# Kernel optimization log

Measured on AMD Instinct MI355X. Metric: run time of the kernel, lower is better.

Reference implementation:

```python
import jax, jax.numpy as jnp
import numpy as np

N = 100000      # nodes per graph-batch
E = 1600000     # edges per graph-batch (avg degree 16)
G = 64          # graphs per batch (segments for mean pool)
DIN = 128
DH = 128


def setup_inputs() -> dict:
    key = jax.random.key(0)
    ks = jax.random.split(key, 14)
    x0 = jax.random.normal(ks[0], (N, DIN), jnp.float32)
    x1 = jax.random.normal(ks[1], (N, DIN), jnp.float32)
    edge_index0 = jax.random.randint(ks[2], (2, E), 0, N)
    edge_index1 = jax.random.randint(ks[3], (2, E), 0, N)
    batch0 = jnp.sort(jax.random.randint(ks[4], (N,), 0, G))
    batch1 = jnp.sort(jax.random.randint(ks[5], (N,), 0, G))
    s = 0.05
    W1 = jax.random.normal(ks[6], (DIN, DH), jnp.float32) * s
    b1 = jnp.zeros((DH,), jnp.float32)
    W2 = jax.random.normal(ks[7], (DH, DH), jnp.float32) * s
    b2 = jnp.zeros((DH,), jnp.float32)
    Wc1 = jax.random.normal(ks[8], (2 * DH, DH), jnp.float32) * s
    bc1 = jnp.zeros((DH,), jnp.float32)
    Wc2 = jax.random.normal(ks[9], (DH, 1), jnp.float32) * s
    bc2 = jnp.zeros((1,), jnp.float32)
    return dict(x0=x0, x1=x1, edge_index0=edge_index0, edge_index1=edge_index1,
                batch0=batch0, batch1=batch1,
                W1=W1, b1=b1, W2=W2, b2=b2, Wc1=Wc1, bc1=bc1, Wc2=Wc2, bc2=bc2)


def gcn_conv(x, edge_index, W, b):
    # PyG GCNConv: add self-loops, symmetric norm D^-1/2 (A+I) D^-1/2, then XW + b
    n = x.shape[0]
    sl = jnp.arange(n)
    src = jnp.concatenate([edge_index[0], sl])
    dst = jnp.concatenate([edge_index[1], sl])
    ones = jnp.ones(src.shape[0], x.dtype)
    deg = jax.ops.segment_sum(ones, dst, num_segments=n)
    dinv = jnp.where(deg > 0, jax.lax.rsqrt(deg), 0.0)
    norm = dinv[src] * dinv[dst]               # [E+N]
    h = x @ W                                   # [N, DH]
    msg = h[src] * norm[:, None]                # gather + scale
    return jax.ops.segment_sum(msg, dst, num_segments=n) + b


def graph_embedding(x, edge_index, batch, W1, b1, W2, b2):
    f = gcn_conv(x, edge_index, W1, b1)
    # dropout is identity in eval mode
    f = gcn_conv(f, edge_index, W2, b2)
    s = jax.ops.segment_sum(f, batch, num_segments=G)
    cnt = jax.ops.segment_sum(jnp.ones((f.shape[0],), f.dtype), batch, num_segments=G)
    return s / jnp.maximum(cnt, 1.0)[:, None]   # global_mean_pool -> [G, DH]


def reference(x0, x1, edge_index0, edge_index1, batch0, batch1,
              W1, b1, W2, b2, Wc1, bc1, Wc2, bc2):
    f0 = graph_embedding(x0, edge_index0, batch0, W1, b1, W2, b2)
    f1 = graph_embedding(x1, edge_index1, batch1, W1, b1, W2, b2)
    c = jnp.concatenate([f0, f1], axis=1)       # [G, 2*DH]
    h = jax.nn.sigmoid(c @ Wc1 + bc1)
    prob = jax.nn.sigmoid(h @ Wc2 + bc2)
    return prob[:, 0]                           # squeeze(-1) -> [G]
```

## Files before the change

### kernel.cpp

```cpp
#include <hip/hip_runtime.h>
#include <hip/hip_bf16.h>

#define NN 100000
#define NE 1600000
#define NG 64
#define DHID 128
#define PB 32
#define NBUCK 196
#define CAPE 10240
#define CHUNK 8192

#if __has_builtin(__builtin_amdgcn_cvt_pk_f32_fp8) && __has_builtin(__builtin_amdgcn_cvt_pk_fp8_f32)
#define FP8_HW 1
#endif

typedef float f32x2 __attribute__((ext_vector_type(2)));
typedef float f32x4 __attribute__((ext_vector_type(4)));
typedef short bf16x8 __attribute__((ext_vector_type(8)));

__device__ __forceinline__ float fp8_dec_sw(unsigned b) {
    unsigned u = ((b & 0x80u) << 24) | ((b & 0x7fu) << 20);
    return __uint_as_float(u) * 0x1p+120f;
}
__device__ __forceinline__ unsigned fp8_enc_sw(float f) {
    unsigned s = (__float_as_uint(f) >> 24) & 0x80u;
    float af = fabsf(f);
    if (!(af > 0x1p-10f)) return s;
    if (af > 448.f) af = 448.f;
    int e; float m = frexpf(af, &e);
    int ee = e + 6;
    unsigned bits;
    if (ee <= 0) {
        int k = (int)rintf(af * 512.0f);
        if (k > 7) k = 7;
        bits = (unsigned)k;
    } else {
        int mm = (int)rintf(m * 16.0f);
        if (mm == 16) { mm = 8; ee += 1; }
        if (ee > 15) { ee = 15; mm = 14; }
        bits = ((unsigned)ee << 3) | (unsigned)(mm - 8);
    }
    return s | bits;
}

__device__ __forceinline__ unsigned short fp8_pack2(float a, float b) {
#ifdef FP8_HW
    return (unsigned short)__builtin_amdgcn_cvt_pk_fp8_f32(a, b, 0, false);
#else
    return (unsigned short)(fp8_enc_sw(a) | (fp8_enc_sw(b) << 8));
#endif
}

__device__ __forceinline__ void fp8_acc4(unsigned u, float& a0, float& a1, float& a2, float& a3) {
#ifdef FP8_HW
    f32x2 lo = __builtin_amdgcn_cvt_pk_f32_fp8((int)u, false);
    f32x2 hi = __builtin_amdgcn_cvt_pk_f32_fp8((int)u, true);
    a0 += lo[0]; a1 += lo[1]; a2 += hi[0]; a3 += hi[1];
#else
    a0 += fp8_dec_sw(u & 0xffu);
    a1 += fp8_dec_sw((u >> 8) & 0xffu);
    a2 += fp8_dec_sw((u >> 16) & 0xffu);
    a3 += fp8_dec_sw(u >> 24);
#endif
}

__device__ __forceinline__ unsigned short f2bf(float f) {
    unsigned u = __float_as_uint(f);
    return (unsigned short)((u + 0x7FFFu + ((u >> 16) & 1u)) >> 16);
}


__global__ void initcur_kernel(int* __restrict__ cursor) {
    int i = blockIdx.x * 256 + threadIdx.x;
    if (i < 2 * NBUCK) cursor[i] = i * CAPE;
}

__global__ __launch_bounds__(256) void bin_kernel(const int* __restrict__ ei0, const int* __restrict__ ei1,
                                                  int* __restrict__ cursor,
                                                  unsigned int* __restrict__ binned, int E, int nch) {
    __shared__ int hist[256], scn[256], lofs[256], lcur[256], basex[256];
    __shared__ unsigned int stage[CHUNK];
    __shared__ unsigned char stageB[CHUNK];
    int g = blockIdx.x / nch;
    int ch = blockIdx.x - g * nch;
    const int* ei = g ? ei1 : ei0;
    int* cur = cursor + g * NBUCK;
    int t = threadIdx.x;
    int c0 = ch * CHUNK;
    int cend = min(c0 + CHUNK, E);
    hist[t] = 0;
    __syncthreads();
    for (int e = c0 + t; e < cend; e += 256)
        atomicAdd(&hist[((unsigned)ei[E + e]) >> 9], 1);
    __syncthreads();
    scn[t] = hist[t];
    __syncthreads();
    for (int off = 1; off < 256; off <<= 1) {
        int v = (t >= off) ? scn[t - off] : 0;
        __syncthreads();
        scn[t] += v;
        __syncthreads();
    }
    int excl = scn[t] - hist[t];
    lofs[t] = excl;
    lcur[t] = excl;
    if (hist[t] > 0) basex[t] = atomicAdd(&cur[t], hist[t]);
    __syncthreads();
    for (int e = c0 + t; e < cend; e += 256) {
        int dst = ei[E + e], src = ei[e];
        int b = ((unsigned)dst) >> 9;
        int r = atomicAdd(&lcur[b], 1);
        stage[r]  = (((unsigned)(dst & 511)) << 17) | (unsigned)src;
        stageB[r] = (unsigned char)b;
    }
    __syncthreads();
    int cnt = cend - c0;
    for (int i = t; i < cnt; i += 256) {
        int b = stageB[i];
        binned[basex[b] + (i - lofs[b])] = stage[i];
    }
}

__global__ __launch_bounds__(256) void fine_kernel(int* __restrict__ cursor,
                                                   unsigned int* __restrict__ binned,
                                                   float* __restrict__ dinv, int2* __restrict__ rng) {
    __shared__ unsigned int stage[CAPE];
    __shared__ int hist[512], ofs[512], lcur[512];
    __shared__ int pscan[256];
    int bb = blockIdx.x;
    int g = bb / NBUCK, bl = bb - g * NBUCK;
    int t = threadIdx.x;
    int gbase = bb * CAPE;
    int cnt = min(cursor[bb] - gbase, CAPE);
    for (int i = t; i < cnt; i += 256) stage[i] = binned[gbase + i];
    hist[t] = 0; hist[t + 256] = 0;
    __syncthreads();
    for (int i = t; i < cnt; i += 256) atomicAdd(&hist[stage[i] >> 17], 1);
    __syncthreads();
    int a0 = hist[2 * t], a1 = hist[2 * t + 1];
    pscan[t] = a0 + a1;
    __syncthreads();
    for (int off = 1; off < 256; off <<= 1) {
        int v = (t >= off) ? pscan[t - off] : 0;
        __syncthreads();
        pscan[t] += v;
        __syncthreads();
    }
    int pex = pscan[t] - (a0 + a1);
    ofs[2 * t] = pex;       ofs[2 * t + 1] = pex + a0;
    lcur[2 * t] = pex;      lcur[2 * t + 1] = pex + a0;
    __syncthreads();
#pragma unroll
    for (int q = 0; q < 2; ++q) {
        int l = t + 256 * q;
        int node = bl * 512 + l;
        if (node < NN) {
            int dg = hist[l];
            dinv[(size_t)g * NN + node] = rsqrtf((float)(dg + 1));
            rng[(size_t)g * NN + node] = make_int2(gbase + ofs[l], gbase + ofs[l] + dg);
        }
    }
    for (int i = t; i < cnt; i += 256) {
        unsigned int p = stage[i];
        int l = p >> 17;
        int r = atomicAdd(&lcur[l], 1);
        binned[gbase + r] = p & 0x1FFFFu;
    }
    if (t == 0) cursor[bb] = gbase;
}


__global__ void bounds_kernel(const int* __restrict__ b0, const int* __restrict__ b1,
                              int* __restrict__ bounds, int n) {
    int t = threadIdx.x;
    int gb = t >> 6, j = t & 63;
    const int* b = gb ? b1 : b0;
    int lo = 0, hi = n;
    while (lo < hi) { int mid = (lo + hi) >> 1; if (b[mid] < j) lo = mid + 1; else hi = mid; }
    bounds[gb * 65 + j] = lo;
    if (j == 0) bounds[gb * 65 + 64] = n;
}


__global__ __launch_bounds__(256) void wpack_kernel(const float* __restrict__ W1, const float* __restrict__ W2,
                                                    unsigned short* __restrict__ Wp1, unsigned short* __restrict__ Wp2) {
    int o = blockIdx.x * 256 + threadIdx.x;
    const float* W = (o < 16384) ? W1 : W2;
    unsigned short* Wp = (o < 16384) ? Wp1 : Wp2;
    int oo = o & 16383;
    int j = oo & 7, l = (oo >> 3) & 63, tile = oo >> 9;
    int kt = tile >> 3, ct = tile & 7;
    int k = kt * 32 + ((l >> 4) << 3) + j;
    int c = ct * 16 + (l & 15);
    Wp[oo] = f2bf(W[k * 128 + c]);
}


template<bool BF16IN>
__global__ __launch_bounds__(256) void gemm_mfma(const void* __restrict__ Avoid,
                                                 const unsigned short* __restrict__ Wp,
                                                 const float* __restrict__ dinv,
                                                 unsigned int* __restrict__ Hs8dw, int n) {
    int wave = threadIdx.x >> 6, lane = threadIdx.x & 63;
    int row_base = blockIdx.x * 64 + wave * 16;
    int r = lane & 15, kg = lane >> 4;
    int rowc = min(row_base + r, n - 1);

    bf16x8 af[4];
    if (BF16IN) {
        const uint4* A = (const uint4*)Avoid;
#pragma unroll
        for (int kt = 0; kt < 4; ++kt) {
            uint4 p = A[(size_t)rowc * 16 + kt * 4 + kg];
            af[kt] = *(bf16x8*)&p;
        }
    } else {
        const float4* A = (const float4*)Avoid;
#pragma unroll
        for (int kt = 0; kt < 4; ++kt) {
            float4 p0 = A[(size_t)rowc * 32 + kt * 8 + kg * 2];
            float4 p1 = A[(size_t)rowc * 32 + kt * 8 + kg * 2 + 1];
            bf16x8 a;
            a[0] = (short)f2bf(p0.x); a[1] = (short)f2bf(p0.y);
            a[2] = (short)f2bf(p0.z); a[3] = (short)f2bf(p0.w);
            a[4] = (short)f2bf(p1.x); a[5] = (short)f2bf(p1.y);
            a[6] = (short)f2bf(p1.z); a[7] = (short)f2bf(p1.w);
            af[kt] = a;
        }
    }

    f32x4 acc[8] = {};
    const bf16x8* Wf = (const bf16x8*)Wp;
#pragma unroll
    for (int kt = 0; kt < 4; ++kt) {
#pragma unroll
        for (int ct = 0; ct < 8; ++ct) {
            bf16x8 bf = Wf[(kt * 8 + ct) * 64 + lane];
            acc[ct] = __builtin_amdgcn_mfma_f32_16x16x32_bf16(af[kt], bf, acc[ct], 0, 0, 0);
        }
    }

    float dvr[4]; bool rok[4]; int erow[4];
#pragma unroll
    for (int reg = 0; reg < 4; ++reg) {
        erow[reg] = row_base + ((lane >> 4) << 2) + reg;
        rok[reg] = erow[reg] < n;
        dvr[reg] = dinv[min(erow[reg], n - 1)];
    }
#pragma unroll
    for (int ct = 0; ct < 8; ++ct) {
#pragma unroll
        for (int reg = 0; reg < 4; ++reg) {
            float v = acc[ct][reg] * dvr[reg];
            float v1 = __shfl_xor(v, 1);
            unsigned us = fp8_pack2(v, v1);
            unsigned u2 = (unsigned)__shfl_xor((int)us, 2);
            if ((lane & 3) == 0 && rok[reg]) {
                unsigned dword = (us & 0xffffu) | (u2 << 16);
                Hs8dw[(size_t)erow[reg] * 32 + ct * 4 + ((lane & 15) >> 2)] = dword;
            }
        }
    }
}


__global__ __launch_bounds__(256) void conv_gather(const unsigned int* __restrict__ Hs8,
                                                   const int2* __restrict__ rng,
                                                   const int* __restrict__ csr, const float* __restrict__ dinv,
                                                   const float* __restrict__ bias, uint2* __restrict__ out16, int n) {
    int wave = blockIdx.x * 4 + (threadIdx.x >> 6);
    int lane = threadIdx.x & 63;
    if (wave >= n) return;
    int d = wave;
    int half = lane >> 5;
    int h = lane & 31;
    int2 se = rng[d];
    int k0 = se.x, k1 = se.y;
    float a0 = 0.f, a1 = 0.f, a2 = 0.f, a3 = 0.f;
    int k = k0 + half;
    for (; k + 14 < k1; k += 16) {
        int s0 = csr[k],      s1 = csr[k + 2],  s2 = csr[k + 4],  s3 = csr[k + 6];
        int s4 = csr[k + 8],  s5 = csr[k + 10], s6 = csr[k + 12], s7 = csr[k + 14];
        unsigned u0 = Hs8[(size_t)s0 * 32 + h];
        unsigned u1 = Hs8[(size_t)s1 * 32 + h];
        unsigned u2 = Hs8[(size_t)s2 * 32 + h];
        unsigned u3 = Hs8[(size_t)s3 * 32 + h];
        unsigned u4 = Hs8[(size_t)s4 * 32 + h];
        unsigned u5 = Hs8[(size_t)s5 * 32 + h];
        unsigned u6 = Hs8[(size_t)s6 * 32 + h];
        unsigned u7 = Hs8[(size_t)s7 * 32 + h];
        fp8_acc4(u0, a0, a1, a2, a3);
        fp8_acc4(u1, a0, a1, a2, a3);
        fp8_acc4(u2, a0, a1, a2, a3);
        fp8_acc4(u3, a0, a1, a2, a3);
        fp8_acc4(u4, a0, a1, a2, a3);
        fp8_acc4(u5, a0, a1, a2, a3);
        fp8_acc4(u6, a0, a1, a2, a3);
        fp8_acc4(u7, a0, a1, a2, a3);
    }
    for (; k + 6 < k1; k += 8) {
        int s0 = csr[k], s1 = csr[k + 2], s2 = csr[k + 4], s3 = csr[k + 6];
        unsigned u0 = Hs8[(size_t)s0 * 32 + h];
        unsigned u1 = Hs8[(size_t)s1 * 32 + h];
        unsigned u2 = Hs8[(size_t)s2 * 32 + h];
        unsigned u3 = Hs8[(size_t)s3 * 32 + h];
        fp8_acc4(u0, a0, a1, a2, a3);
        fp8_acc4(u1, a0, a1, a2, a3);
        fp8_acc4(u2, a0, a1, a2, a3);
        fp8_acc4(u3, a0, a1, a2, a3);
    }
    for (; k < k1; k += 2) {
        unsigned u = Hs8[(size_t)csr[k] * 32 + h];
        fp8_acc4(u, a0, a1, a2, a3);
    }
    if (half == 0) {
        unsigned ud = Hs8[(size_t)d * 32 + h];
        fp8_acc4(ud, a0, a1, a2, a3);
    }
    a0 += __shfl_xor(a0, 32);
    a1 += __shfl_xor(a1, 32);
    a2 += __shfl_xor(a2, 32);
    a3 += __shfl_xor(a3, 32);
    if (half == 0) {
        float dv = dinv[d];
        float4 b = ((const float4*)bias)[h];
        unsigned short w0 = f2bf(fmaf(a0, dv, b.x));
        unsigned short w1 = f2bf(fmaf(a1, dv, b.y));
        unsigned short w2 = f2bf(fmaf(a2, dv, b.z));
        unsigned short w3 = f2bf(fmaf(a3, dv, b.w));
        uint2 o;
        o.x = (unsigned)w0 | ((unsigned)w1 << 16);
        o.y = (unsigned)w2 | ((unsigned)w3 << 16);
        out16[(size_t)d * 32 + h] = o;
    }
}


__global__ __launch_bounds__(256) void pool_part(const unsigned int* __restrict__ F16,
                                                 const int* __restrict__ bounds,
                                                 float* __restrict__ partial) {
    __shared__ float sh[512];
    int g   = blockIdx.x / PB;
    int sub = blockIdx.x % PB;
    int s = bounds[g], e = bounds[g + 1];
    int len = e - s;
    int chunk = (len + PB - 1) / PB;
    int is = s + sub * chunk;
    int ie = min(is + chunk, e);
    int cp = threadIdx.x & 63;
    int quarter = threadIdx.x >> 6;
    float acc0 = 0.f, acc1 = 0.f;
    for (int i = is + quarter; i < ie; i += 4) {
        unsigned u = F16[(size_t)i * 64 + cp];
        acc0 += __uint_as_float(u << 16);
        acc1 += __uint_as_float(u & 0xffff0000u);
    }
    sh[threadIdx.x] = acc0;
    sh[threadIdx.x + 256] = acc1;
    __syncthreads();
    if (threadIdx.x < 64) {
        float m0 = sh[cp] + sh[64 + cp] + sh[128 + cp] + sh[192 + cp];
        float m1 = sh[256 + cp] + sh[320 + cp] + sh[384 + cp] + sh[448 + cp];
        partial[((size_t)g * PB + sub) * 128 + 2 * cp]     = m0;
        partial[((size_t)g * PB + sub) * 128 + 2 * cp + 1] = m1;
    }
}


__global__ __launch_bounds__(128) void pool_finish(const float* __restrict__ partial, const int* __restrict__ bounds,
                                                   float* __restrict__ pool) {
    int gg = blockIdx.x;
    int gb = gg >> 6, g = gg & 63;
    int col = threadIdx.x;
    const float* p = partial + ((size_t)gb * NG + g) * PB * 128;
    float acc = 0.f;
#pragma unroll
    for (int sub = 0; sub < PB; ++sub) acc += p[sub * 128 + col];
    int len = bounds[gb * 65 + g + 1] - bounds[gb * 65 + g];
    pool[(size_t)gg * 128 + col] = acc / fmaxf((float)len, 1.0f);
}


__global__ __launch_bounds__(128) void classifier_kernel(const float* __restrict__ pool,
                                                         const float* __restrict__ Wc1, const float* __restrict__ bc1,
                                                         const float* __restrict__ Wc2, const float* __restrict__ bc2,
                                                         float* __restrict__ out) {
    __shared__ float sh[128];
    int g = blockIdx.x;
    int j = threadIdx.x;
    float acc = bc1[j];
    const float* p0 = pool + (size_t)g * 128;
    const float* p1 = pool + (size_t)(NG + g) * 128;
    for (int k = 0; k < 128; ++k) acc = fmaf(p0[k], Wc1[k * 128 + j], acc);
    for (int k = 0; k < 128; ++k) acc = fmaf(p1[k], Wc1[(128 + k) * 128 + j], acc);
    float h = 1.0f / (1.0f + expf(-acc));
    sh[j] = h * Wc2[j];
    __syncthreads();
    for (int off = 64; off > 0; off >>= 1) {
        if (j < off) sh[j] += sh[j + off];
        __syncthreads();
    }
    if (j == 0) out[g] = 1.0f / (1.0f + expf(-(sh[0] + bc2[0])));
}


extern "C" void kernel_launch(void* const* d_in, const int* in_sizes, int n_in,
                              void* d_out, int out_size, void* d_ws, size_t ws_size,
                              hipStream_t stream) {
    const float* x[2]     = {(const float*)d_in[0], (const float*)d_in[1]};
    const int*   ei[2]    = {(const int*)d_in[2], (const int*)d_in[3]};
    const int*   batch[2] = {(const int*)d_in[4], (const int*)d_in[5]};
    const float* W1  = (const float*)d_in[6];
    const float* b1  = (const float*)d_in[7];
    const float* W2  = (const float*)d_in[8];
    const float* b2  = (const float*)d_in[9];
    const float* Wc1 = (const float*)d_in[10];
    const float* bc1 = (const float*)d_in[11];
    const float* Wc2 = (const float*)d_in[12];
    const float* bc2 = (const float*)d_in[13];
    float* out = (float*)d_out;

    char* w = (char*)d_ws;
    unsigned short*  buf16  = (unsigned short*)w;  w += (size_t)NN * DHID * 2;
    unsigned short*  hs     = (unsigned short*)w;  w += (size_t)NN * DHID;
    unsigned int*    binned = (unsigned int*)w;    w += (size_t)2 * NBUCK * CAPE * 4;
    int2*            rng    = (int2*)w;            w += (size_t)2 * NN * 8;
    float*           dinv   = (float*)w;           w += (size_t)2 * NN * 4;
    unsigned short*  wp1    = (unsigned short*)w;  w += (size_t)128 * 128 * 2;
    unsigned short*  wp2    = (unsigned short*)w;  w += (size_t)128 * 128 * 2;
    int*             cursor = (int*)w;             w += (size_t)2 * NBUCK * 4 + 16;
    int*             bounds = (int*)w;             w += 2 * 65 * 4 + 8;
    float*           partial= (float*)w;           w += (size_t)2 * NG * PB * DHID * 4;
    float*           pool   = (float*)w;           w += (size_t)2 * NG * DHID * 4;

    if ((size_t)(w - (char*)d_ws) > ws_size) return;

    const int nch = (NE + CHUNK - 1) / CHUNK;

    bounds_kernel<<<1, 128, 0, stream>>>(batch[0], batch[1], bounds, NN);
    wpack_kernel<<<128, 256, 0, stream>>>(W1, W2, wp1, wp2);
    initcur_kernel<<<2, 256, 0, stream>>>(cursor);

    bin_kernel<<<2 * nch, 256, 0, stream>>>(ei[0], ei[1], cursor, binned, NE, nch);
    fine_kernel<<<2 * NBUCK, 256, 0, stream>>>(cursor, binned, dinv, rng);

    const int gemm_grid = (NN + 63) / 64;

    for (int g = 0; g < 2; ++g) {
        const float* dv = dinv + (size_t)g * NN;
        const int2*  rg = rng + (size_t)g * NN;

        gemm_mfma<false><<<gemm_grid, 256, 0, stream>>>(x[g], wp1, dv, (unsigned int*)hs, NN);
        conv_gather<<<(NN + 3) / 4, 256, 0, stream>>>((const unsigned int*)hs, rg, (const int*)binned, dv, b1, (uint2*)buf16, NN);
        gemm_mfma<true><<<gemm_grid, 256, 0, stream>>>(buf16, wp2, dv, (unsigned int*)hs, NN);
        conv_gather<<<(NN + 3) / 4, 256, 0, stream>>>((const unsigned int*)hs, rg, (const int*)binned, dv, b2, (uint2*)buf16, NN);

        pool_part<<<NG * PB, 256, 0, stream>>>((const unsigned int*)buf16, bounds + g * 65, partial + (size_t)g * NG * PB * DHID);
    }

    pool_finish<<<2 * NG, 128, 0, stream>>>(partial, bounds, pool);
    classifier_kernel<<<NG, 128, 0, stream>>>(pool, Wc1, bc1, Wc2, bc2, out);
}
```

Baseline: 387.3 us.

## Batch both graphs per GEMM launch and permute hidden columns to drop epilogue shuffles

```diff
diff --git a/kernel.cpp b/kernel.cpp
--- a/kernel.cpp
+++ b/kernel.cpp
@@ -17,6 +17,8 @@
 typedef float f32x2 __attribute__((ext_vector_type(2)));
 typedef float f32x4 __attribute__((ext_vector_type(4)));
 typedef short bf16x8 __attribute__((ext_vector_type(8)));
+
+#define PERM(b) ((((b) & 7) << 4) | ((b) >> 3))
 
 __device__ __forceinline__ float fp8_dec_sw(unsigned b) {
     unsigned u = ((b & 0x80u) << 24) | ((b & 0x7fu) << 20);
@@ -69,6 +71,16 @@
     return (unsigned short)((u + 0x7FFFu + ((u >> 16) & 1u)) >> 16);
 }
 
+__device__ __forceinline__ unsigned cvt_pk_bf16(float a, float b) {
+#if defined(__AMDGCN__)
+    unsigned r;
+    asm("v_cvt_pk_bf16_f32 %0, %1, %2" : "=v"(r) : "v"(a), "v"(b));
+    return r;
+#else
+    return (unsigned)f2bf(a) | ((unsigned)f2bf(b) << 16);
+#endif
+}
+
 
 __global__ void initcur_kernel(int* __restrict__ cursor) {
     int i = blockIdx.x * 256 + threadIdx.x;
@@ -185,48 +197,48 @@
 __global__ __launch_bounds__(256) void wpack_kernel(const float* __restrict__ W1, const float* __restrict__ W2,
                                                     unsigned short* __restrict__ Wp1, unsigned short* __restrict__ Wp2) {
     int o = blockIdx.x * 256 + threadIdx.x;
-    const float* W = (o < 16384) ? W1 : W2;
-    unsigned short* Wp = (o < 16384) ? Wp1 : Wp2;
+    bool second = o >= 16384;
+    const float* W = second ? W2 : W1;
+    unsigned short* Wp = second ? Wp2 : Wp1;
     int oo = o & 16383;
     int j = oo & 7, l = (oo >> 3) & 63, tile = oo >> 9;
     int kt = tile >> 3, ct = tile & 7;
-    int k = kt * 32 + ((l >> 4) << 3) + j;
+    int kk = kt * 32 + ((l >> 4) << 3) + j;
+    int k = second ? PERM(kk) : kk;
     int c = ct * 16 + (l & 15);
     Wp[oo] = f2bf(W[k * 128 + c]);
 }
 
-
-template<bool BF16IN>
-__global__ __launch_bounds__(256) void gemm_mfma(const void* __restrict__ Avoid,
-                                                 const unsigned short* __restrict__ Wp,
-                                                 const float* __restrict__ dinv,
-                                                 unsigned int* __restrict__ Hs8dw, int n) {
+__global__ void pbias_kernel(const float* __restrict__ b1, const float* __restrict__ b2, float* __restrict__ pb) {
+    int t = threadIdx.x;
+    int g = t >> 7, i = t & 127;
+    pb[g * 128 + i] = (g ? b2 : b1)[PERM(i)];
+}
+
+
+__global__ __launch_bounds__(256) void gemm_f32(const float* __restrict__ x0, const float* __restrict__ x1,
+                                                const unsigned short* __restrict__ Wp,
+                                                const float* __restrict__ dinv,
+                                                uint2* __restrict__ Hs8, int nblk) {
+    int g = blockIdx.x >= nblk;
+    int bl = blockIdx.x - g * nblk;
+    const float4* A = (const float4*)(g ? x1 : x0);
     int wave = threadIdx.x >> 6, lane = threadIdx.x & 63;
-    int row_base = blockIdx.x * 64 + wave * 16;
+    int row_base = bl * 64 + wave * 16;
     int r = lane & 15, kg = lane >> 4;
-    int rowc = min(row_base + r, n - 1);
+    int rowc = min(row_base + r, NN - 1);
 
     bf16x8 af[4];
-    if (BF16IN) {
-        const uint4* A = (const uint4*)Avoid;
-#pragma unroll
-        for (int kt = 0; kt < 4; ++kt) {
-            uint4 p = A[(size_t)rowc * 16 + kt * 4 + kg];
-            af[kt] = *(bf16x8*)&p;
-        }
-    } else {
-        const float4* A = (const float4*)Avoid;
-#pragma unroll
-        for (int kt = 0; kt < 4; ++kt) {
-            float4 p0 = A[(size_t)rowc * 32 + kt * 8 + kg * 2];
-            float4 p1 = A[(size_t)rowc * 32 + kt * 8 + kg * 2 + 1];
-            bf16x8 a;
-            a[0] = (short)f2bf(p0.x); a[1] = (short)f2bf(p0.y);
-            a[2] = (short)f2bf(p0.z); a[3] = (short)f2bf(p0.w);
-            a[4] = (short)f2bf(p1.x); a[5] = (short)f2bf(p1.y);
-            a[6] = (short)f2bf(p1.z); a[7] = (short)f2bf(p1.w);
-            af[kt] = a;
-        }
+#pragma unroll
+    for (int kt = 0; kt < 4; ++kt) {
+        float4 p0 = A[(size_t)rowc * 32 + kt * 8 + kg * 2];
+        float4 p1 = A[(size_t)rowc * 32 + kt * 8 + kg * 2 + 1];
+        unsigned d0 = cvt_pk_bf16(p0.x, p0.y);
+        unsigned d1 = cvt_pk_bf16(p0.z, p0.w);
+        unsigned d2 = cvt_pk_bf16(p1.x, p1.y);
+        unsigned d3 = cvt_pk_bf16(p1.z, p1.w);
+        uint4 q = make_uint4(d0, d1, d2, d3);
+        af[kt] = *(bf16x8*)&q;
     }
 
     f32x4 acc[8] = {};
@@ -240,25 +252,64 @@
         }
     }
 
-    float dvr[4]; bool rok[4]; int erow[4];
 #pragma unroll
     for (int reg = 0; reg < 4; ++reg) {
-        erow[reg] = row_base + ((lane >> 4) << 2) + reg;
-        rok[reg] = erow[reg] < n;
-        dvr[reg] = dinv[min(erow[reg], n - 1)];
-    }
-#pragma unroll
-    for (int ct = 0; ct < 8; ++ct) {
-#pragma unroll
-        for (int reg = 0; reg < 4; ++reg) {
-            float v = acc[ct][reg] * dvr[reg];
-            float v1 = __shfl_xor(v, 1);
-            unsigned us = fp8_pack2(v, v1);
-            unsigned u2 = (unsigned)__shfl_xor((int)us, 2);
-            if ((lane & 3) == 0 && rok[reg]) {
-                unsigned dword = (us & 0xffffu) | (u2 << 16);
-                Hs8dw[(size_t)erow[reg] * 32 + ct * 4 + ((lane & 15) >> 2)] = dword;
-            }
+        int erow = row_base + (kg << 2) + reg;
+        if (erow < NN) {
+            float dv = dinv[(size_t)g * NN + erow];
+            unsigned short p01 = fp8_pack2(acc[0][reg] * dv, acc[1][reg] * dv);
+            unsigned short p23 = fp8_pack2(acc[2][reg] * dv, acc[3][reg] * dv);
+            unsigned short p45 = fp8_pack2(acc[4][reg] * dv, acc[5][reg] * dv);
+            unsigned short p67 = fp8_pack2(acc[6][reg] * dv, acc[7][reg] * dv);
+            uint2 o;
+            o.x = (unsigned)p01 | ((unsigned)p23 << 16);
+            o.y = (unsigned)p45 | ((unsigned)p67 << 16);
+            Hs8[(size_t)(g * NN + erow) * 16 + r] = o;
+        }
+    }
+}
+
+
+__global__ __launch_bounds__(256) void gemm_bf16(const uint4* __restrict__ A,
+                                                 const unsigned short* __restrict__ Wp,
+                                                 const float* __restrict__ dinv,
+                                                 uint2* __restrict__ Hs8, int n2) {
+    int wave = threadIdx.x >> 6, lane = threadIdx.x & 63;
+    int row_base = blockIdx.x * 64 + wave * 16;
+    int r = lane & 15, kg = lane >> 4;
+    int rowc = min(row_base + r, n2 - 1);
+
+    bf16x8 af[4];
+#pragma unroll
+    for (int kt = 0; kt < 4; ++kt) {
+        uint4 p = A[(size_t)rowc * 16 + kt * 4 + kg];
+        af[kt] = *(bf16x8*)&p;
+    }
+
+    f32x4 acc[8] = {};
+    const bf16x8* Wf = (const bf16x8*)Wp;
+#pragma unroll
+    for (int kt = 0; kt < 4; ++kt) {
+#pragma unroll
+        for (int ct = 0; ct < 8; ++ct) {
+            bf16x8 bf = Wf[(kt * 8 + ct) * 64 + lane];
+            acc[ct] = __builtin_amdgcn_mfma_f32_16x16x32_bf16(af[kt], bf, acc[ct], 0, 0, 0);
+        }
+    }
+
+#pragma unroll
+    for (int reg = 0; reg < 4; ++reg) {
+        int erow = row_base + (kg << 2) + reg;
+        if (erow < n2) {
+            float dv = dinv[erow];
+            unsigned short p01 = fp8_pack2(acc[0][reg] * dv, acc[1][reg] * dv);
+            unsigned short p23 = fp8_pack2(acc[2][reg] * dv, acc[3][reg] * dv);
+            unsigned short p45 = fp8_pack2(acc[4][reg] * dv, acc[5][reg] * dv);
+            unsigned short p67 = fp8_pack2(acc[6][reg] * dv, acc[7][reg] * dv);
+            uint2 o;
+            o.x = (unsigned)p01 | ((unsigned)p23 << 16);
+            o.y = (unsigned)p45 | ((unsigned)p67 << 16);
+            Hs8[(size_t)erow * 16 + r] = o;
         }
     }
 }
@@ -267,7 +318,8 @@
 __global__ __launch_bounds__(256) void conv_gather(const unsigned int* __restrict__ Hs8,
                                                    const int2* __restrict__ rng,
                                                    const int* __restrict__ csr, const float* __restrict__ dinv,
-                                                   const float* __restrict__ bias, uint2* __restrict__ out16, int n) {
+                                                   const float* __restrict__ pbias,
+                                                   unsigned long long* __restrict__ out16, int n) {
     int wave = blockIdx.x * 4 + (threadIdx.x >> 6);
     int lane = threadIdx.x & 63;
     if (wave >= n) return;
@@ -279,8 +331,14 @@
     float a0 = 0.f, a1 = 0.f, a2 = 0.f, a3 = 0.f;
     int k = k0 + half;
     for (; k + 14 < k1; k += 16) {
-        int s0 = csr[k],      s1 = csr[k + 2],  s2 = csr[k + 4],  s3 = csr[k + 6];
-        int s4 = csr[k + 8],  s5 = csr[k + 10], s6 = csr[k + 12], s7 = csr[k + 14];
+        int s0 = __builtin_nontemporal_load(&csr[k]);
+        int s1 = __builtin_nontemporal_load(&csr[k + 2]);
+        int s2 = __builtin_nontemporal_load(&csr[k + 4]);
+        int s3 = __builtin_nontemporal_load(&csr[k + 6]);
+        int s4 = __builtin_nontemporal_load(&csr[k + 8]);
+        int s5 = __builtin_nontemporal_load(&csr[k + 10]);
+        int s6 = __builtin_nontemporal_load(&csr[k + 12]);
+        int s7 = __builtin_nontemporal_load(&csr[k + 14]);
         unsigned u0 = Hs8[(size_t)s0 * 32 + h];
         unsigned u1 = Hs8[(size_t)s1 * 32 + h];
         unsigned u2 = Hs8[(size_t)s2 * 32 + h];
@@ -299,7 +357,10 @@
         fp8_acc4(u7, a0, a1, a2, a3);
     }
     for (; k + 6 < k1; k += 8) {
-        int s0 = csr[k], s1 = csr[k + 2], s2 = csr[k + 4], s3 = csr[k + 6];
+        int s0 = __builtin_nontemporal_load(&csr[k]);
+        int s1 = __builtin_nontemporal_load(&csr[k + 2]);
+        int s2 = __builtin_nontemporal_load(&csr[k + 4]);
+        int s3 = __builtin_nontemporal_load(&csr[k + 6]);
         unsigned u0 = Hs8[(size_t)s0 * 32 + h];
         unsigned u1 = Hs8[(size_t)s1 * 32 + h];
         unsigned u2 = Hs8[(size_t)s2 * 32 + h];
@@ -310,7 +371,7 @@
         fp8_acc4(u3, a0, a1, a2, a3);
     }
     for (; k < k1; k += 2) {
-        unsigned u = Hs8[(size_t)csr[k] * 32 + h];
+        unsigned u = Hs8[(size_t)__builtin_nontemporal_load(&csr[k]) * 32 + h];
         fp8_acc4(u, a0, a1, a2, a3);
     }
     if (half == 0) {
@@ -323,15 +384,11 @@
     a3 += __shfl_xor(a3, 32);
     if (half == 0) {
         float dv = dinv[d];
-        float4 b = ((const float4*)bias)[h];
-        unsigned short w0 = f2bf(fmaf(a0, dv, b.x));
-        unsigned short w1 = f2bf(fmaf(a1, dv, b.y));
-        unsigned short w2 = f2bf(fmaf(a2, dv, b.z));
-        unsigned short w3 = f2bf(fmaf(a3, dv, b.w));
-        uint2 o;
-        o.x = (unsigned)w0 | ((unsigned)w1 << 16);
-        o.y = (unsigned)w2 | ((unsigned)w3 << 16);
-        out16[(size_t)d * 32 + h] = o;
+        float4 b = ((const float4*)pbias)[h];
+        unsigned lo = cvt_pk_bf16(fmaf(a0, dv, b.x), fmaf(a1, dv, b.y));
+        unsigned hi = cvt_pk_bf16(fmaf(a2, dv, b.z), fmaf(a3, dv, b.w));
+        unsigned long long o = (unsigned long long)lo | ((unsigned long long)hi << 32);
+        __builtin_nontemporal_store(o, &out16[(size_t)d * 32 + h]);
     }
 }
 
@@ -340,18 +397,22 @@
                                                  const int* __restrict__ bounds,
                                                  float* __restrict__ partial) {
     __shared__ float sh[512];
-    int g   = blockIdx.x / PB;
-    int sub = blockIdx.x % PB;
-    int s = bounds[g], e = bounds[g + 1];
+    int bid = blockIdx.x;
+    int gb  = bid / (NG * PB);
+    int rem = bid - gb * NG * PB;
+    int gseg = rem / PB;
+    int sub  = rem % PB;
+    int s = bounds[gb * 65 + gseg], e = bounds[gb * 65 + gseg + 1];
     int len = e - s;
     int chunk = (len + PB - 1) / PB;
     int is = s + sub * chunk;
     int ie = min(is + chunk, e);
     int cp = threadIdx.x & 63;
     int quarter = threadIdx.x >> 6;
+    size_t rbase = (size_t)gb * NN;
     float acc0 = 0.f, acc1 = 0.f;
     for (int i = is + quarter; i < ie; i += 4) {
-        unsigned u = F16[(size_t)i * 64 + cp];
+        unsigned u = F16[(rbase + i) * 64 + cp];
         acc0 += __uint_as_float(u << 16);
         acc1 += __uint_as_float(u & 0xffff0000u);
     }
@@ -361,8 +422,8 @@
     if (threadIdx.x < 64) {
         float m0 = sh[cp] + sh[64 + cp] + sh[128 + cp] + sh[192 + cp];
         float m1 = sh[256 + cp] + sh[320 + cp] + sh[384 + cp] + sh[448 + cp];
-        partial[((size_t)g * PB + sub) * 128 + 2 * cp]     = m0;
-        partial[((size_t)g * PB + sub) * 128 + 2 * cp + 1] = m1;
+        partial[((size_t)(gb * NG + gseg) * PB + sub) * 128 + 2 * cp]     = m0;
+        partial[((size_t)(gb * NG + gseg) * PB + sub) * 128 + 2 * cp + 1] = m1;
     }
 }
 
@@ -391,8 +452,8 @@
     float acc = bc1[j];
     const float* p0 = pool + (size_t)g * 128;
     const float* p1 = pool + (size_t)(NG + g) * 128;
-    for (int k = 0; k < 128; ++k) acc = fmaf(p0[k], Wc1[k * 128 + j], acc);
-    for (int k = 0; k < 128; ++k) acc = fmaf(p1[k], Wc1[(128 + k) * 128 + j], acc);
+    for (int b = 0; b < 128; ++b) acc = fmaf(p0[b], Wc1[PERM(b) * 128 + j], acc);
+    for (int b = 0; b < 128; ++b) acc = fmaf(p1[b], Wc1[(128 + PERM(b)) * 128 + j], acc);
     float h = 1.0f / (1.0f + expf(-acc));
     sh[j] = h * Wc2[j];
     __syncthreads();
@@ -421,13 +482,14 @@
     float* out = (float*)d_out;
 
     char* w = (char*)d_ws;
-    unsigned short*  buf16  = (unsigned short*)w;  w += (size_t)NN * DHID * 2;
-    unsigned short*  hs     = (unsigned short*)w;  w += (size_t)NN * DHID;
+    unsigned short*  buf16  = (unsigned short*)w;  w += (size_t)2 * NN * DHID * 2;
+    unsigned char*   hs     = (unsigned char*)w;   w += (size_t)2 * NN * DHID;
     unsigned int*    binned = (unsigned int*)w;    w += (size_t)2 * NBUCK * CAPE * 4;
     int2*            rng    = (int2*)w;            w += (size_t)2 * NN * 8;
     float*           dinv   = (float*)w;           w += (size_t)2 * NN * 4;
     unsigned short*  wp1    = (unsigned short*)w;  w += (size_t)128 * 128 * 2;
     unsigned short*  wp2    = (unsigned short*)w;  w += (size_t)128 * 128 * 2;
+    float*           pb     = (float*)w;           w += 2 * 128 * 4;
     int*             cursor = (int*)w;             w += (size_t)2 * NBUCK * 4 + 16;
     int*             bounds = (int*)w;             w += 2 * 65 * 4 + 8;
     float*           partial= (float*)w;           w += (size_t)2 * NG * PB * DHID * 4;
@@ -439,25 +501,29 @@
 
     bounds_kernel<<<1, 128, 0, stream>>>(batch[0], batch[1], bounds, NN);
     wpack_kernel<<<128, 256, 0, stream>>>(W1, W2, wp1, wp2);
+    pbias_kernel<<<1, 256, 0, stream>>>(b1, b2, pb);
     initcur_kernel<<<2, 256, 0, stream>>>(cursor);
 
     bin_kernel<<<2 * nch, 256, 0, stream>>>(ei[0], ei[1], cursor, binned, NE, nch);
     fine_kernel<<<2 * NBUCK, 256, 0, stream>>>(cursor, binned, dinv, rng);
 
-    const int gemm_grid = (NN + 63) / 64;
-
-    for (int g = 0; g < 2; ++g) {
-        const float* dv = dinv + (size_t)g * NN;
-        const int2*  rg = rng + (size_t)g * NN;
-
-        gemm_mfma<false><<<gemm_grid, 256, 0, stream>>>(x[g], wp1, dv, (unsigned int*)hs, NN);
-        conv_gather<<<(NN + 3) / 4, 256, 0, stream>>>((const unsigned int*)hs, rg, (const int*)binned, dv, b1, (uint2*)buf16, NN);
-        gemm_mfma<true><<<gemm_grid, 256, 0, stream>>>(buf16, wp2, dv, (unsigned int*)hs, NN);
-        conv_gather<<<(NN + 3) / 4, 256, 0, stream>>>((const unsigned int*)hs, rg, (const int*)binned, dv, b2, (uint2*)buf16, NN);
-
-        pool_part<<<NG * PB, 256, 0, stream>>>((const unsigned int*)buf16, bounds + g * 65, partial + (size_t)g * NG * PB * DHID);
-    }
-
+    const int nblk = (NN + 63) / 64;
+    const int conv_grid = (NN + 3) / 4;
+
+    gemm_f32<<<2 * nblk, 256, 0, stream>>>(x[0], x[1], wp1, dinv, (uint2*)hs, nblk);
+    for (int g = 0; g < 2; ++g)
+        conv_gather<<<conv_grid, 256, 0, stream>>>((const unsigned int*)(hs + (size_t)g * NN * DHID),
+                                                   rng + (size_t)g * NN, (const int*)binned,
+                                                   dinv + (size_t)g * NN, pb,
+                                                   (unsigned long long*)(buf16 + (size_t)g * NN * DHID), NN);
+    gemm_bf16<<<(2 * NN + 63) / 64, 256, 0, stream>>>((const uint4*)buf16, wp2, dinv, (uint2*)hs, 2 * NN);
+    for (int g = 0; g < 2; ++g)
+        conv_gather<<<conv_grid, 256, 0, stream>>>((const unsigned int*)(hs + (size_t)g * NN * DHID),
+                                                   rng + (size_t)g * NN, (const int*)binned,
+                                                   dinv + (size_t)g * NN, pb + 128,
+                                                   (unsigned long long*)(buf16 + (size_t)g * NN * DHID), NN);
+
+    pool_part<<<2 * NG * PB, 256, 0, stream>>>((const unsigned int*)buf16, bounds, partial);
     pool_finish<<<2 * NG, 128, 0, stream>>>(partial, bounds, pool);
     classifier_kernel<<<NG, 128, 0, stream>>>(pool, Wc1, bc1, Wc2, bc2, out);
 }
```

New measurement: 415.9 us. 7.4% more time.
